# Kernel optimization log

Hardware: AMD Instinct MI355X
Metric: run time of the kernel (lower is better)

The kernel has to match this reference:

```python
import jax, jax.numpy as jnp
import numpy as np

N, CIN, T, V = 64, 192, 256, 25
K, COUT, S = 3, 64, 5  # kernel_size, out_channels, num_semantic


def setup_inputs() -> dict:
    key = jax.random.key(0)
    ks = jax.random.split(key, 8)
    x = jax.random.normal(ks[0], (N, CIN, T, V), jnp.float32)
    A = jax.random.normal(ks[1], (K, V, V), jnp.float32)
    node_type = jnp.arange(V, dtype=jnp.int64) % S  # every semantic type present
    Wc = jax.random.normal(ks[2], (COUT * K, CIN), jnp.float32) * 0.02
    bc = jax.random.normal(ks[3], (COUT * K,), jnp.float32) * 0.02
    W1 = jax.random.normal(ks[4], (S * COUT, COUT * K), jnp.float32) * 0.02
    b1 = jax.random.normal(ks[5], (S * COUT,), jnp.float32) * 0.02
    W2 = jax.random.normal(ks[6], (S * COUT, COUT * K), jnp.float32) * 0.02
    b2 = jax.random.normal(ks[7], (S * COUT,), jnp.float32) * 0.02
    return {"x": x, "A": A, "node_type": node_type, "Wc": Wc, "bc": bc,
            "W1": W1, "b1": b1, "W2": W2, "b2": b2}


def reference(x, A, node_type, Wc, bc, W1, b1, W2, b2):
    # self.conv: 1x1 conv (t_kernel_size=1) -> (N, K*COUT, T, V)
    y = jnp.einsum('nctv,oc->notv', x, Wc) + bc[None, :, None, None]
    # conv1 / conv2 applied to tmp_x = y, reshape to (N, S, COUT, T, V), mean over T
    x1 = (jnp.einsum('nctv,oc->notv', y, W1) + b1[None, :, None, None]).reshape(N, S, COUT, T, V)
    x2 = (jnp.einsum('nctv,oc->notv', y, W2) + b2[None, :, None, None]).reshape(N, S, COUT, T, V)
    x1 = x1.mean(axis=3, keepdims=True)  # (N, S, COUT, 1, V)
    x2 = x2.mean(axis=3, keepdims=True)  # (N, S, COUT, 1, V)
    # per-semantic masked mean over nodes (vectorized over the 5 semantic types)
    masks = (node_type[None, :] == jnp.arange(S)[:, None]).astype(y.dtype)  # (S, V)
    counts = masks.sum(axis=-1)  # (S,)
    sem = jnp.einsum('nsclv,sv->nscl', x1, masks) / counts[None, :, None, None]  # (N,S,COUT,1)
    # diff: (N, S, COUT, 1, 1, V)  (graph_list stacked over the semantic axis)
    graphs = sem[..., None, None] - x2[:, :, :, :, None, :]
    # graph conv with adjacency A
    xk = y.reshape(N, K, COUT, T, V)
    out = jnp.einsum('nkctv,kvw->nctw', xk, A)  # (N, COUT, T, V)
    return out, A, graphs
```

## Files before the change

### kernel.cpp

```cpp
#include <hip/hip_runtime.h>

#define N_    64
#define CIN_  192
#define T_    256
#define V_    25
#define K_    3
#define COUT_ 64
#define OC_   192
#define SS_   5

#define OUT_OFF_A (N_*COUT_*T_*V_)
#define OUT_OFF_G (OUT_OFF_A + K_*V_*V_)

#define TCH   4
#define HCH   2
#define NCOLS 100
#define XB_STRIDE 200
#define YB_STRIDE 104
#define UNION_SHORTS 26624
#define NYV  4800
#define NBLK (N_*(T_/(TCH*HCH)))

typedef __attribute__((ext_vector_type(8))) short short8;
typedef __attribute__((ext_vector_type(4))) float float4v;

__device__ inline unsigned bf16r(float f) {
    unsigned u = __float_as_uint(f);
    return (u + 0x7fffu + ((u >> 16) & 1u)) >> 16;
}

__global__ __launch_bounds__(256) void prep(const float* __restrict__ Wc,
                                            const float* __restrict__ A,
                                            short* __restrict__ WcB,
                                            short* __restrict__ A2T,
                                            float* __restrict__ out) {
    int idx = blockIdx.x * 256 + threadIdx.x;
    if (idx < OC_ * CIN_) WcB[idx] = (short)bf16r(Wc[idx]);
    if (idx < 32 * YB_STRIDE) {
        int w = idx / YB_STRIDE, kk = idx - w * YB_STRIDE;
        short val = 0;
        if (w < V_ && kk < K_ * V_) {
            int k = kk / V_, v = kk - k * V_;
            val = (short)bf16r(A[k * V_ * V_ + v * V_ + w]);
        }
        A2T[idx] = val;
    }
    if (idx < K_ * V_ * V_) out[OUT_OFF_A + idx] = A[idx];
}

__global__ __launch_bounds__(256, 2) void fused_mfma(const float* __restrict__ x,
                                                     const short* __restrict__ WcB,
                                                     const float* __restrict__ bc,
                                                     const short* __restrict__ A2T,
                                                     float* __restrict__ out,
                                                     float* __restrict__ part) {
    __shared__ __align__(16) short U[UNION_SHORTS];
    __shared__ __align__(16) short A2l[32 * YB_STRIDE];

    const int tid  = threadIdx.x;
    const int lane = tid & 63;
    const int wv   = tid >> 6;
    const int l15  = lane & 15;
    const int q    = lane >> 4;
    const int n    = blockIdx.x >> 5;
    const int tc   = blockIdx.x & 31;

    for (int i = tid; i < 32 * YB_STRIDE / 2; i += 256)
        ((int*)A2l)[i] = ((const int*)A2T)[i];

    short8 wfrag[3][6];
    const int rt0 = wv * 3;
    {
        const short* wb = WcB + (rt0 * 16 + l15) * CIN_ + q * 8;
#pragma unroll
        for (int j = 0; j < 3; ++j)
#pragma unroll
            for (int ks = 0; ks < 6; ++ks)
                wfrag[j][ks] = *(const short8*)(wb + j * 16 * CIN_ + ks * 32);
    }
    float4v bvec[3];
#pragma unroll
    for (int j = 0; j < 3; ++j)
        bvec[j] = *(const float4v*)(bc + (rt0 + j) * 16 + q * 4);

    float racc[19];
#pragma unroll
    for (int u = 0; u < 19; ++u) racc[u] = 0.f;

    for (int h = 0; h < HCH; ++h) {
        const int t0 = tc * (TCH * HCH) + h * TCH;
        __syncthreads();

        const float* xn = x + (size_t)n * (CIN_ * T_ * V_) + t0 * V_;
        for (int i = tid; i < CIN_ * (NCOLS / 4); i += 256) {
            int c    = i / (NCOLS / 4);
            int col4 = i - c * (NCOLS / 4);
            float4 xv = ((const float4*)(xn + c * (T_ * V_)))[col4];
            U[(col4 * 4 + 0) * XB_STRIDE + c] = (short)bf16r(xv.x);
            U[(col4 * 4 + 1) * XB_STRIDE + c] = (short)bf16r(xv.y);
            U[(col4 * 4 + 2) * XB_STRIDE + c] = (short)bf16r(xv.z);
            U[(col4 * 4 + 3) * XB_STRIDE + c] = (short)bf16r(xv.w);
        }
        __syncthreads();

        float4v acc[3][7];
#pragma unroll
        for (int j = 0; j < 3; ++j)
#pragma unroll
            for (int ct = 0; ct < 7; ++ct) acc[j][ct] = bvec[j];

#pragma unroll
        for (int ct = 0; ct < 7; ++ct) {
            const short* xb = &U[(ct * 16 + l15) * XB_STRIDE + q * 8];
#pragma unroll
            for (int ks = 0; ks < 6; ++ks) {
                short8 bfrag = *(const short8*)(xb + ks * 32);
#pragma unroll
                for (int j = 0; j < 3; ++j)
                    acc[j][ct] = __builtin_amdgcn_mfma_f32_16x16x32_bf16(
                        wfrag[j][ks], bfrag, acc[j][ct], 0, 0, 0);
            }
        }
        __syncthreads();

        {
            int4 z = make_int4(0, 0, 0, 0);
            for (int i = tid; i < UNION_SHORTS / 8; i += 256) ((int4*)U)[i] = z;
        }
        __syncthreads();

#pragma unroll
        for (int ct = 0; ct < 7; ++ct) {
            int col = ct * 16 + l15;
            if (col < NCOLS) {
                int tl = col / V_;
                int v  = col - tl * V_;
#pragma unroll
                for (int j = 0; j < 3; ++j) {
                    int obase = (rt0 + j) * 16 + q * 4;
#pragma unroll
                    for (int i = 0; i < 4; ++i) {
                        int o   = obase + i;
                        int row = tl * 64 + (o & 63);
                        int cY  = (o >> 6) * V_ + v;
                        U[row * YB_STRIDE + cY] = (short)bf16r(acc[j][ct][i]);
                    }
                }
            }
        }
        __syncthreads();

        short8 b2[2][3];
#pragma unroll
        for (int nt = 0; nt < 2; ++nt)
#pragma unroll
            for (int ks = 0; ks < 3; ++ks)
                b2[nt][ks] = *(const short8*)&A2l[(nt * 16 + l15) * YB_STRIDE + ks * 32 + q * 8];

        float4v o2[4][2];
#pragma unroll
        for (int mt = 0; mt < 4; ++mt)
#pragma unroll
            for (int nt = 0; nt < 2; ++nt) o2[mt][nt] = (float4v){0.f, 0.f, 0.f, 0.f};

#pragma unroll
        for (int mt = 0; mt < 4; ++mt) {
            int m = (wv * 4 + mt) * 16 + l15;
            const short* yb = &U[m * YB_STRIDE + q * 8];
#pragma unroll
            for (int ks = 0; ks < 3; ++ks) {
                short8 af = *(const short8*)(yb + ks * 32);
#pragma unroll
                for (int nt = 0; nt < 2; ++nt)
                    o2[mt][nt] = __builtin_amdgcn_mfma_f32_16x16x32_bf16(
                        af, b2[nt][ks], o2[mt][nt], 0, 0, 0);
            }
        }

#pragma unroll
        for (int mt = 0; mt < 4; ++mt) {
#pragma unroll
            for (int nt = 0; nt < 2; ++nt) {
                int w = nt * 16 + l15;
                if (w < V_) {
#pragma unroll
                    for (int i = 0; i < 4; ++i) {
                        int m  = (wv * 4 + mt) * 16 + q * 4 + i;
                        int cc = m & 63, tl = m >> 6;
                        out[((size_t)(n * COUT_ + cc) * T_ + (t0 + tl)) * V_ + w] = o2[mt][nt][i];
                    }
                }
            }
        }

#pragma unroll
        for (int u = 0; u < 19; ++u) {
            int idx = tid + u * 256;
            if (u < 18 || idx < NYV) {
                int o = idx / V_, v = idx - (idx / V_) * V_;
                int cc = o & 63, k = o >> 6;
                const short* yp = &U[cc * YB_STRIDE + k * V_ + v];
                float s = 0.f;
#pragma unroll
                for (int tl = 0; tl < TCH; ++tl) {
                    unsigned b = (unsigned short)yp[tl * 64 * YB_STRIDE];
                    s += __uint_as_float(b << 16);
                }
                racc[u] += s;
            }
        }
    }

    float* pb = part + (size_t)blockIdx.x * NYV;
#pragma unroll
    for (int u = 0; u < 19; ++u) {
        int idx = tid + u * 256;
        if (u < 18 || idx < NYV) pb[idx] = racc[u];
    }
}

__global__ __launch_bounds__(256) void yred(const float* __restrict__ part,
                                            float* __restrict__ ysum) {
    int i = blockIdx.x * 256 + threadIdx.x;
    if (i >= N_ * NYV) return;
    int n = i / NYV;
    int r = i - n * NYV;
    const float* p = part + (size_t)n * 32 * NYV + r;
    float s = 0.f;
#pragma unroll
    for (int tc = 0; tc < 32; ++tc) s += p[tc * NYV];
    ysum[i] = s * (1.0f / T_);
}

__global__ __launch_bounds__(256) void e2_graphs(const float* __restrict__ ysum,
                                                 const float* __restrict__ W1,
                                                 const float* __restrict__ b1,
                                                 const float* __restrict__ W2,
                                                 const float* __restrict__ b2,
                                                 const int* __restrict__ node_type,
                                                 float* __restrict__ out) {
    __shared__ float s1[10][V_];
    __shared__ float sem[10];
    const int tid = threadIdx.x;
    const int n  = blockIdx.x >> 5;
    const int jc = blockIdx.x & 31;
    const int jl = tid / V_;
    const int v  = tid - jl * V_;
    const int j  = jc * 10 + jl;
    float x2 = 0.f;
    if (jl < 10) {
        const float* yb = ysum + (size_t)n * NYV + v;
        const float* w1 = W1 + j * OC_;
        const float* w2 = W2 + j * OC_;
        float a1 = b1[j], a2 = b2[j];
        for (int o = 0; o < OC_; ++o) {
            float yv = yb[o * V_];
            a1 += w1[o] * yv;
            a2 += w2[o] * yv;
        }
        s1[jl][v] = a1;
        x2 = a2;
    }
    __syncthreads();
    if (tid < 10) {
        int s = (jc * 10 + tid) >> 6;
        float sum = 0.f, cnt = 0.f;
        for (int vv = 0; vv < V_; ++vv)
            if (node_type[vv] == s) { sum += s1[tid][vv]; cnt += 1.f; }
        sem[tid] = sum / cnt;
    }
    __syncthreads();
    if (jl < 10)
        out[OUT_OFF_G + (size_t)n * (SS_ * COUT_ * V_) + j * V_ + v] = sem[jl] - x2;
}

extern "C" void kernel_launch(void* const* d_in, const int* in_sizes, int n_in,
                              void* d_out, int out_size, void* d_ws, size_t ws_size,
                              hipStream_t stream) {
    const float* x         = (const float*)d_in[0];
    const float* A         = (const float*)d_in[1];
    const int*   node_type = (const int*)d_in[2];
    const float* Wc        = (const float*)d_in[3];
    const float* bc        = (const float*)d_in[4];
    const float* W1        = (const float*)d_in[5];
    const float* b1        = (const float*)d_in[6];
    const float* W2        = (const float*)d_in[7];
    const float* b2        = (const float*)d_in[8];
    float* out = (float*)d_out;

    float* part = (float*)d_ws;
    float* ysum = part + (size_t)NBLK * NYV;
    short* WcB  = (short*)(ysum + N_ * NYV);
    short* A2T  = WcB + OC_ * CIN_;

    hipLaunchKernelGGL(prep, dim3((OC_ * CIN_ + 255) / 256), dim3(256), 0, stream,
                       Wc, A, WcB, A2T, out);
    hipLaunchKernelGGL(fused_mfma, dim3(NBLK), dim3(256), 0, stream,
                       x, WcB, bc, A2T, out, part);
    hipLaunchKernelGGL(yred, dim3((N_ * NYV + 255) / 256), dim3(256), 0, stream,
                       part, ysum);
    hipLaunchKernelGGL(e2_graphs, dim3(N_ * 32), dim3(256), 0, stream,
                       ysum, W1, b1, W2, b2, node_type, out);
}
```

Measured before the change: 664.5 us.

## Double per-block time chunks, vectorize x staging, drop per-iteration LDS zeroing

```diff
diff --git a/kernel.cpp b/kernel.cpp
--- a/kernel.cpp
+++ b/kernel.cpp
@@ -13,13 +13,15 @@
 #define OUT_OFF_G (OUT_OFF_A + K_*V_*V_)
 
 #define TCH   4
-#define HCH   2
+#define HCH   4
 #define NCOLS 100
 #define XB_STRIDE 200
 #define YB_STRIDE 104
 #define UNION_SHORTS 26624
 #define NYV  4800
-#define NBLK (N_*(T_/(TCH*HCH)))
+#define CPN  (T_/(TCH*HCH))
+#define NBLK (N_*CPN)
+#define CHUNK_UNITS ((CIN_/8)*NCOLS)
 
 typedef __attribute__((ext_vector_type(8))) short short8;
 typedef __attribute__((ext_vector_type(4))) float float4v;
@@ -55,18 +57,19 @@
                                                      float* __restrict__ out,
                                                      float* __restrict__ part) {
     __shared__ __align__(16) short U[UNION_SHORTS];
-    __shared__ __align__(16) short A2l[32 * YB_STRIDE];
 
     const int tid  = threadIdx.x;
     const int lane = tid & 63;
     const int wv   = tid >> 6;
     const int l15  = lane & 15;
     const int q    = lane >> 4;
-    const int n    = blockIdx.x >> 5;
-    const int tc   = blockIdx.x & 31;
-
-    for (int i = tid; i < 32 * YB_STRIDE / 2; i += 256)
-        ((int*)A2l)[i] = ((const int*)A2T)[i];
+    const int n    = blockIdx.x >> 4;
+    const int tc   = blockIdx.x & 15;
+
+    {
+        int4 z = make_int4(0, 0, 0, 0);
+        for (int i = tid; i < UNION_SHORTS / 8; i += 256) ((int4*)U)[i] = z;
+    }
 
     short8 wfrag[3][6];
     const int rt0 = wv * 3;
@@ -78,10 +81,6 @@
             for (int ks = 0; ks < 6; ++ks)
                 wfrag[j][ks] = *(const short8*)(wb + j * 16 * CIN_ + ks * 32);
     }
-    float4v bvec[3];
-#pragma unroll
-    for (int j = 0; j < 3; ++j)
-        bvec[j] = *(const float4v*)(bc + (rt0 + j) * 16 + q * 4);
 
     float racc[19];
 #pragma unroll
@@ -92,22 +91,29 @@
         __syncthreads();
 
         const float* xn = x + (size_t)n * (CIN_ * T_ * V_) + t0 * V_;
-        for (int i = tid; i < CIN_ * (NCOLS / 4); i += 256) {
-            int c    = i / (NCOLS / 4);
-            int col4 = i - c * (NCOLS / 4);
-            float4 xv = ((const float4*)(xn + c * (T_ * V_)))[col4];
-            U[(col4 * 4 + 0) * XB_STRIDE + c] = (short)bf16r(xv.x);
-            U[(col4 * 4 + 1) * XB_STRIDE + c] = (short)bf16r(xv.y);
-            U[(col4 * 4 + 2) * XB_STRIDE + c] = (short)bf16r(xv.z);
-            U[(col4 * 4 + 3) * XB_STRIDE + c] = (short)bf16r(xv.w);
+        for (int u = tid; u < CHUNK_UNITS; u += 256) {
+            int col = u % NCOLS;
+            int cg  = u / NCOLS;
+            const float* xp = xn + (size_t)cg * 8 * (T_ * V_) + col;
+            short8 s;
+#pragma unroll
+            for (int j = 0; j < 8; ++j)
+                s[j] = (short)bf16r(xp[(size_t)j * (T_ * V_)]);
+            *(short8*)&U[col * XB_STRIDE + cg * 8] = s;
         }
         __syncthreads();
 
         float4v acc[3][7];
-#pragma unroll
-        for (int j = 0; j < 3; ++j)
-#pragma unroll
-            for (int ct = 0; ct < 7; ++ct) acc[j][ct] = bvec[j];
+        {
+            float4v bvec[3];
+#pragma unroll
+            for (int j = 0; j < 3; ++j)
+                bvec[j] = *(const float4v*)(bc + (rt0 + j) * 16 + q * 4);
+#pragma unroll
+            for (int j = 0; j < 3; ++j)
+#pragma unroll
+                for (int ct = 0; ct < 7; ++ct) acc[j][ct] = bvec[j];
+        }
 
 #pragma unroll
         for (int ct = 0; ct < 7; ++ct) {
@@ -120,12 +126,6 @@
                     acc[j][ct] = __builtin_amdgcn_mfma_f32_16x16x32_bf16(
                         wfrag[j][ks], bfrag, acc[j][ct], 0, 0, 0);
             }
-        }
-        __syncthreads();
-
-        {
-            int4 z = make_int4(0, 0, 0, 0);
-            for (int i = tid; i < UNION_SHORTS / 8; i += 256) ((int4*)U)[i] = z;
         }
         __syncthreads();
 
@@ -155,7 +155,7 @@
         for (int nt = 0; nt < 2; ++nt)
 #pragma unroll
             for (int ks = 0; ks < 3; ++ks)
-                b2[nt][ks] = *(const short8*)&A2l[(nt * 16 + l15) * YB_STRIDE + ks * 32 + q * 8];
+                b2[nt][ks] = *(const short8*)&A2T[(nt * 16 + l15) * YB_STRIDE + ks * 32 + q * 8];
 
         float4v o2[4][2];
 #pragma unroll
@@ -225,10 +225,10 @@
     if (i >= N_ * NYV) return;
     int n = i / NYV;
     int r = i - n * NYV;
-    const float* p = part + (size_t)n * 32 * NYV + r;
+    const float* p = part + (size_t)n * CPN * NYV + r;
     float s = 0.f;
 #pragma unroll
-    for (int tc = 0; tc < 32; ++tc) s += p[tc * NYV];
+    for (int tc = 0; tc < CPN; ++tc) s += p[tc * NYV];
     ysum[i] = s * (1.0f / T_);
 }
 
```

Measured after the change: 637.5 us. 4.1% less time.
